# Kernel tuning notes

Measured on AMD Instinct MI355X. Metric: run time of the kernel, lower is better.

## Reference

```python
import jax, jax.numpy as jnp
import numpy as np

D_MODEL = 512
NUM_HEADS = 8
NUM_REL_EMB = 1024


def _linear(x, w, b):
    # torch nn.Linear convention: w is [out, in]
    return x @ w.T + b


def setup_inputs() -> dict:
    key = jax.random.key(0)
    B, S, D = 1, 512, D_MODEL
    ks = jax.random.split(key, 14)
    scale = D ** -0.5
    def w(i):
        return jax.random.normal(ks[i], (D, D), jnp.float32) * scale
    def b(i):
        return jax.random.normal(ks[i], (D,), jnp.float32) * 0.01
    return {
        "hidden_states": jax.random.normal(ks[0], (B, S, D), jnp.float32),
        "emb_table": jax.random.normal(ks[1], (NUM_REL_EMB, D), jnp.float32) * 0.02,
        "wq": w(2), "bq": b(3),
        "wk": w(4), "bk": b(5),
        "wv": w(6), "bv": b(7),
        "wrk": w(8), "brk": b(9),
        "wrq": w(10), "brq": b(11),
        "wo": w(12), "bo": b(13),
    }


def reference(hidden_states, emb_table, wq, bq, wk, bk, wv, bv,
              wrk, brk, wrq, brq, wo, bo):
    B, S, D = hidden_states.shape
    H = NUM_HEADS
    hd = D // H
    NE = emb_table.shape[0]

    # relative positions j - i, shifted and clamped, then embedded: [S, S, D]
    rel_pos = jnp.arange(S)[None, :] - jnp.arange(S)[:, None]
    idx = jnp.clip(rel_pos + NE // 2, 0, NE - 1)
    rel_emb = emb_table[idx]  # [S, S, D] (identical across batch)

    q = _linear(hidden_states, wq, bq).reshape(B, S, H, hd).transpose(0, 2, 1, 3)  # [B,H,S,hd]
    k = _linear(hidden_states, wk, bk).reshape(B, S, H, hd).transpose(0, 2, 1, 3)
    v = _linear(hidden_states, wv, bv).reshape(B, S, H, hd).transpose(0, 2, 1, 3)

    rk = _linear(rel_emb, wrk, brk).reshape(S, S, H, hd)  # [i, j, H, hd]
    rq = _linear(rel_emb, wrq, brq).reshape(S, S, H, hd)

    # content-content + content-relative + relative-content scores: [B,H,S,S]
    scores = (
        jnp.einsum('bhid,bhjd->bhij', q, k)
        + jnp.einsum('bhid,ijhd->bhij', q, rk)
        + jnp.einsum('ijhd,bhjd->bhij', rq, k)
    )

    attn = jax.nn.softmax(scores / jnp.sqrt(jnp.asarray(hd, scores.dtype)), axis=-1)
    # dropout is identity (p=0.0 / eval mode)

    ctx = jnp.einsum('bhij,bhjd->bhid', attn, v)          # [B,H,S,hd]
    ctx = ctx.transpose(0, 2, 1, 3).reshape(B, S, D)       # merge heads
    out = _linear(ctx, wo, bo)
    return out, attn
```

## Files before the change

### kernel.cpp

```cpp
#include <hip/hip_runtime.h>
#include <stdint.h>


typedef __bf16 bf16_t;
typedef bf16_t bf16x8 __attribute__((ext_vector_type(8)));
typedef float f32x4 __attribute__((ext_vector_type(4)));

__device__ __forceinline__ uint16_t f2bf(float f) {
  union { float f; uint32_t i; } c; c.f = f;
  return (uint16_t)((c.i + 0x7fffu + ((c.i >> 16) & 1u)) >> 16);
}
__device__ __forceinline__ uint32_t pack2bf(float lo, float hi) {
  return (uint32_t)f2bf(lo) | ((uint32_t)f2bf(hi) << 16);
}
#define MFMA(a, b, c) __builtin_amdgcn_mfma_f32_16x16x32_bf16((a), (b), (c), 0, 0, 0)

#define LSTR 40
#define SSTR 72

__global__ __launch_bounds__(256) void gemm_bt_kernel(
    const void* __restrict__ A, int lda, int zsA, int aF32,
    const void* __restrict__ B, int ldb, int zsB, int bF32,
    const float* __restrict__ bias, int hasBias,
    float* __restrict__ C, int ldc, int zsC, int K)
{
  __shared__ __align__(16) uint16_t As[64 * LSTR];
  __shared__ __align__(16) uint16_t Bs[64 * LSTR];
  const int z = blockIdx.z;
  const int m0 = blockIdx.y * 64, n0 = blockIdx.x * 64;
  const int t = threadIdx.x, lane = t & 63, wave = t >> 6;
  const int wi = wave & 1, wj = wave >> 1;
  const int quad = lane >> 4, l15 = lane & 15;
  const int srow = t >> 2, scol = (t & 3) * 8;

  f32x4 acc[2][2] = {};
  for (int k0 = 0; k0 < K; k0 += 32) {
    uint4 ap, bp;
    if (aF32) {
      const float* Af = (const float*)A + (size_t)z * zsA + (size_t)(m0 + srow) * lda + (k0 + scol);
      float4 x0 = *(const float4*)(Af); float4 x1 = *(const float4*)(Af + 4);
      ap.x = pack2bf(x0.x, x0.y); ap.y = pack2bf(x0.z, x0.w);
      ap.z = pack2bf(x1.x, x1.y); ap.w = pack2bf(x1.z, x1.w);
    } else {
      ap = *(const uint4*)((const uint16_t*)A + (size_t)z * zsA + (size_t)(m0 + srow) * lda + (k0 + scol));
    }
    if (bF32) {
      const float* Bf = (const float*)B + (size_t)z * zsB + (size_t)(n0 + srow) * ldb + (k0 + scol);
      float4 x0 = *(const float4*)(Bf); float4 x1 = *(const float4*)(Bf + 4);
      bp.x = pack2bf(x0.x, x0.y); bp.y = pack2bf(x0.z, x0.w);
      bp.z = pack2bf(x1.x, x1.y); bp.w = pack2bf(x1.z, x1.w);
    } else {
      bp = *(const uint4*)((const uint16_t*)B + (size_t)z * zsB + (size_t)(n0 + srow) * ldb + (k0 + scol));
    }
    *(uint4*)(&As[srow * LSTR + scol]) = ap;
    *(uint4*)(&Bs[srow * LSTR + scol]) = bp;
    __syncthreads();
    bf16x8 af[2], bfr[2];
#pragma unroll
    for (int x = 0; x < 2; x++) {
      af[x]  = *(const bf16x8*)(&As[(wi * 32 + x * 16 + l15) * LSTR + quad * 8]);
      bfr[x] = *(const bf16x8*)(&Bs[(wj * 32 + x * 16 + l15) * LSTR + quad * 8]);
    }
#pragma unroll
    for (int x = 0; x < 2; x++)
#pragma unroll
      for (int y = 0; y < 2; y++)
        acc[x][y] = MFMA(af[x], bfr[y], acc[x][y]);
    __syncthreads();
  }
#pragma unroll
  for (int x = 0; x < 2; x++)
#pragma unroll
    for (int y = 0; y < 2; y++) {
      const int j = n0 + wj * 32 + y * 16 + l15;
      const float bval = hasBias ? bias[j] : 0.0f;
      const int ib = m0 + wi * 32 + x * 16 + quad * 4;
#pragma unroll
      for (int r = 0; r < 4; r++)
        C[(size_t)z * zsC + (size_t)(ib + r) * ldc + j] = acc[x][y][r] + bval;
    }
}

__global__ __launch_bounds__(256) void proj_kernel(
    const float* __restrict__ X, const float* __restrict__ emb,
    const float* __restrict__ wq, const float* __restrict__ bq,
    const float* __restrict__ wk, const float* __restrict__ bk,
    const float* __restrict__ wv, const float* __restrict__ bv,
    const float* __restrict__ wrk, const float* __restrict__ brk,
    const float* __restrict__ wrq, const float* __restrict__ brq,
    uint16_t* __restrict__ q, uint16_t* __restrict__ k, uint16_t* __restrict__ vT,
    uint16_t* __restrict__ rkE, uint16_t* __restrict__ rqE)
{
  int bid = blockIdx.x;
  const float *A, *B, *bias; uint16_t* C; int mode;
  if (bid < 64)       {            A = X;   B = wq;  bias = bq;  C = q;   mode = 2; }
  else if (bid < 128) { bid -= 64; A = X;   B = wk;  bias = bk;  C = k;   mode = 2; }
  else if (bid < 192) { bid -= 128; A = X;  B = wv;  bias = bv;  C = vT;  mode = 3; }
  else if (bid < 320) { bid -= 192; A = emb; B = wrk; bias = brk; C = rkE; mode = 1; }
  else                { bid -= 320; A = emb; B = wrq; bias = brq; C = rqE; mode = 1; }
  const int m0 = (bid >> 3) * 64, n0 = (bid & 7) * 64;

  __shared__ __align__(16) uint16_t As[64 * LSTR];
  __shared__ __align__(16) uint16_t Bs[64 * LSTR];
  const int t = threadIdx.x, lane = t & 63, wave = t >> 6;
  const int wi = wave & 1, wj = wave >> 1;
  const int quad = lane >> 4, l15 = lane & 15;
  const int srow = t >> 2, scol = (t & 3) * 8;

  f32x4 acc[2][2] = {};
  for (int k0 = 0; k0 < 512; k0 += 32) {
    const float* Af = A + (size_t)(m0 + srow) * 512 + (k0 + scol);
    const float* Bf = B + (size_t)(n0 + srow) * 512 + (k0 + scol);
    float4 a0 = *(const float4*)(Af), a1 = *(const float4*)(Af + 4);
    float4 b0 = *(const float4*)(Bf), b1 = *(const float4*)(Bf + 4);
    uint4 ap, bp;
    ap.x = pack2bf(a0.x, a0.y); ap.y = pack2bf(a0.z, a0.w);
    ap.z = pack2bf(a1.x, a1.y); ap.w = pack2bf(a1.z, a1.w);
    bp.x = pack2bf(b0.x, b0.y); bp.y = pack2bf(b0.z, b0.w);
    bp.z = pack2bf(b1.x, b1.y); bp.w = pack2bf(b1.z, b1.w);
    *(uint4*)(&As[srow * LSTR + scol]) = ap;
    *(uint4*)(&Bs[srow * LSTR + scol]) = bp;
    __syncthreads();
    bf16x8 af[2], bfr[2];
#pragma unroll
    for (int x = 0; x < 2; x++) {
      af[x]  = *(const bf16x8*)(&As[(wi * 32 + x * 16 + l15) * LSTR + quad * 8]);
      bfr[x] = *(const bf16x8*)(&Bs[(wj * 32 + x * 16 + l15) * LSTR + quad * 8]);
    }
#pragma unroll
    for (int x = 0; x < 2; x++)
#pragma unroll
      for (int y = 0; y < 2; y++)
        acc[x][y] = MFMA(af[x], bfr[y], acc[x][y]);
    __syncthreads();
  }
#pragma unroll
  for (int x = 0; x < 2; x++)
#pragma unroll
    for (int y = 0; y < 2; y++) {
      const int j = n0 + wj * 32 + y * 16 + l15;
      const float bval = bias[j];
      const int ib = m0 + wi * 32 + x * 16 + quad * 4;
#pragma unroll
      for (int r = 0; r < 4; r++) {
        const int i = ib + r;
        size_t off;
        if (mode == 1)      off = (size_t)i * 512 + j;
        else if (mode == 2) off = (size_t)(j >> 6) * 32768 + (size_t)i * 64 + (size_t)(j & 63);
        else                off = (size_t)(j >> 6) * 32768 + (size_t)(j & 63) * 512 + (size_t)i;
        C[off] = f2bf(acc[x][y][r] + bval);
      }
    }
}

__global__ __launch_bounds__(256, 1) void attn_fused_kernel(
    const uint16_t* __restrict__ q, const uint16_t* __restrict__ k,
    const uint16_t* __restrict__ rkE, const uint16_t* __restrict__ rqE,
    const uint16_t* __restrict__ vT,
    float* __restrict__ attn, uint16_t* __restrict__ ctx_bf)
{
  __shared__ __align__(16) char smem[131840];
  const int h = blockIdx.y, i0 = blockIdx.x * 16;
  const int t = threadIdx.x, lane = t & 63, w = t >> 6;
  const int quad = lane >> 4, l15 = lane & 15;

  uint16_t* stgw = (uint16_t*)smem + w * 16128;
  float* U2f  = (float*)stgw;
  float* U3f  = (float*)((char*)stgw + 5376);
  uint16_t* Pw = stgw;
  float* ctxw = (float*)((char*)stgw + 8192);
  uint16_t* qs = (uint16_t*)(smem + 129024);
  float* rmax = (float*)(smem + 131328);
  float* rsum = rmax + 64;

  if (t < 128) {
    const int row = t >> 3, col = (t & 7) * 8;
    *(uint4*)(&qs[row * SSTR + col]) =
        *(const uint4*)(q + (size_t)h * 32768 + (size_t)(i0 + row) * 64 + col);
  }

  f32x4 sc[2][4];
  const int jbase = w * 2;
#pragma unroll
  for (int jt2 = 0; jt2 < 2; jt2++) {
    const int j0 = (jbase + jt2) * 64;
    const int ebase = j0 - i0 + 497;
    __syncthreads();
#pragma unroll
    for (int c = 0; c < 28; c++) {
      const int idx = lane + c * 64;
      const int row = idx >> 3, col = (idx & 7) * 8;
      const uint16_t* src;
      if (row < 64)       src = k   + (size_t)h * 32768 + (size_t)(j0 + row) * 64 + col;
      else if (row < 144) src = rqE + (size_t)min(ebase + row - 64, 1023) * 512 + h * 64 + col;
      else                src = rkE + (size_t)min(ebase + row - 144, 1023) * 512 + h * 64 + col;
      *(uint4*)(&stgw[row * SSTR + col]) = *(const uint4*)src;
    }
    __syncthreads();

    f32x4 acc1[4] = {}, acc2[5] = {}, acc3[5][4] = {};
#pragma unroll
    for (int s = 0; s < 2; s++) {
      const int ko = s * 32 + quad * 8;
      bf16x8 aq = *(const bf16x8*)(&qs[l15 * SSTR + ko]);
      bf16x8 bk[4], arq[5], brk[5];
#pragma unroll
      for (int tt = 0; tt < 4; tt++) bk[tt]  = *(const bf16x8*)(&stgw[(tt * 16 + l15) * SSTR + ko]);
#pragma unroll
      for (int x = 0; x < 5; x++)    arq[x]  = *(const bf16x8*)(&stgw[(64 + x * 16 + l15) * SSTR + ko]);
#pragma unroll
      for (int x = 0; x < 5; x++)    brk[x]  = *(const bf16x8*)(&stgw[(144 + x * 16 + l15) * SSTR + ko]);
#pragma unroll
      for (int tt = 0; tt < 4; tt++) acc1[tt] = MFMA(aq, bk[tt], acc1[tt]);
#pragma unroll
      for (int x = 0; x < 5; x++)    acc2[x] = MFMA(aq, brk[x], acc2[x]);
#pragma unroll
      for (int x = 0; x < 5; x++)
#pragma unroll
        for (int tt = 0; tt < 4; tt++) acc3[x][tt] = MFMA(arq[x], bk[tt], acc3[x][tt]);
    }
    __syncthreads();
#pragma unroll
    for (int x = 0; x < 5; x++)
#pragma unroll
      for (int r = 0; r < 4; r++)
        U2f[(quad * 4 + r) * 84 + x * 16 + l15] = acc2[x][r];
#pragma unroll
    for (int x = 0; x < 5; x++)
#pragma unroll
      for (int tt = 0; tt < 4; tt++)
#pragma unroll
        for (int r = 0; r < 4; r++)
          U3f[(x * 16 + quad * 4 + r) * 68 + tt * 16 + l15] = acc3[x][tt][r];
    __syncthreads();
#pragma unroll
    for (int tt = 0; tt < 4; tt++)
#pragma unroll
      for (int r = 0; r < 4; r++) {
        const int ii = quad * 4 + r, jj = tt * 16 + l15;
        const int rb = jj - ii + 15;
        sc[jt2][tt][r] = (acc1[tt][r] + U2f[ii * 84 + rb] + U3f[rb * 68 + jj]) * 0.125f;
      }
  }

  float mrow[4], srow[4];
#pragma unroll
  for (int r = 0; r < 4; r++) {
    float m = -1e30f;
#pragma unroll
    for (int jt2 = 0; jt2 < 2; jt2++)
#pragma unroll
      for (int tt = 0; tt < 4; tt++) m = fmaxf(m, sc[jt2][tt][r]);
#pragma unroll
    for (int o = 1; o < 16; o <<= 1) m = fmaxf(m, __shfl_xor(m, o, 64));
    mrow[r] = m;
  }
  if (l15 == 0)
#pragma unroll
    for (int r = 0; r < 4; r++) rmax[w * 16 + quad * 4 + r] = mrow[r];
  __syncthreads();
#pragma unroll
  for (int r = 0; r < 4; r++) {
    const int row = quad * 4 + r;
    const float m = fmaxf(fmaxf(rmax[row], rmax[16 + row]), fmaxf(rmax[32 + row], rmax[48 + row]));
    float s = 0.f;
#pragma unroll
    for (int jt2 = 0; jt2 < 2; jt2++)
#pragma unroll
      for (int tt = 0; tt < 4; tt++) {
        const float p = __expf(sc[jt2][tt][r] - m);
        sc[jt2][tt][r] = p; s += p;
      }
#pragma unroll
    for (int o = 1; o < 16; o <<= 1) s += __shfl_xor(s, o, 64);
    srow[r] = s;
  }
  if (l15 == 0)
#pragma unroll
    for (int r = 0; r < 4; r++) rsum[w * 16 + quad * 4 + r] = srow[r];
  __syncthreads();
#pragma unroll
  for (int r = 0; r < 4; r++) {
    const int row = quad * 4 + r;
    const float inv = 1.0f / (rsum[row] + rsum[16 + row] + rsum[32 + row] + rsum[48 + row]);
#pragma unroll
    for (int jt2 = 0; jt2 < 2; jt2++)
#pragma unroll
      for (int tt = 0; tt < 4; tt++) {
        sc[jt2][tt][r] *= inv;
        attn[((size_t)h * 512 + i0 + row) * 512 + (jbase + jt2) * 64 + tt * 16 + l15]
            = sc[jt2][tt][r];
      }
  }

  f32x4 apv[4] = {};
#pragma unroll
  for (int jt2 = 0; jt2 < 2; jt2++) {
    __syncthreads();
#pragma unroll
    for (int tt = 0; tt < 4; tt++)
#pragma unroll
      for (int r = 0; r < 4; r++)
        Pw[(quad * 4 + r) * SSTR + tt * 16 + l15] = f2bf(sc[jt2][tt][r]);
    __syncthreads();
#pragma unroll
    for (int s = 0; s < 2; s++) {
      const int ko = s * 32 + quad * 8;
      bf16x8 aP = *(const bf16x8*)(&Pw[l15 * SSTR + ko]);
#pragma unroll
      for (int tt = 0; tt < 4; tt++) {
        bf16x8 bv = *(const bf16x8*)(vT + (size_t)h * 32768 + (size_t)(tt * 16 + l15) * 512
                                     + (jbase + jt2) * 64 + ko);
        apv[tt] = MFMA(aP, bv, apv[tt]);
      }
    }
  }
#pragma unroll
  for (int tt = 0; tt < 4; tt++)
#pragma unroll
    for (int r = 0; r < 4; r++)
      ctxw[(quad * 4 + r) * 64 + tt * 16 + l15] = apv[tt][r];
  __syncthreads();
  {
    const int row = t >> 4, col = (t & 15) * 4;
    const size_t off = (size_t)(row * 64 + col) * 4;
    float4 s0 = *(const float4*)(smem + 0 * 32256 + 8192 + off);
    float4 s1 = *(const float4*)(smem + 1 * 32256 + 8192 + off);
    float4 s2 = *(const float4*)(smem + 2 * 32256 + 8192 + off);
    float4 s3 = *(const float4*)(smem + 3 * 32256 + 8192 + off);
    const float c0 = s0.x + s1.x + s2.x + s3.x;
    const float c1 = s0.y + s1.y + s2.y + s3.y;
    const float c2 = s0.z + s1.z + s2.z + s3.z;
    const float c3 = s0.w + s1.w + s2.w + s3.w;
    uint2 pk; pk.x = pack2bf(c0, c1); pk.y = pack2bf(c2, c3);
    *(uint2*)(ctx_bf + (size_t)(i0 + row) * 512 + h * 64 + col) = pk;
  }
}

extern "C" void kernel_launch(void* const* d_in, const int* in_sizes, int n_in,
                              void* d_out, int out_size, void* d_ws, size_t ws_size,
                              hipStream_t stream) {
  const float* X   = (const float*)d_in[0];
  const float* emb = (const float*)d_in[1];
  const float* wq  = (const float*)d_in[2];
  const float* bq  = (const float*)d_in[3];
  const float* wk  = (const float*)d_in[4];
  const float* bk  = (const float*)d_in[5];
  const float* wv  = (const float*)d_in[6];
  const float* bv  = (const float*)d_in[7];
  const float* wrk = (const float*)d_in[8];
  const float* brk = (const float*)d_in[9];
  const float* wrq = (const float*)d_in[10];
  const float* brq = (const float*)d_in[11];
  const float* wo  = (const float*)d_in[12];
  const float* bo  = (const float*)d_in[13];

  uint16_t* q      = (uint16_t*)d_ws;
  uint16_t* k      = q   + 262144;
  uint16_t* vT     = k   + 262144;
  uint16_t* rkE    = vT  + 262144;
  uint16_t* rqE    = rkE + 524288;
  uint16_t* ctx_bf = rqE + 524288;

  float* outp = (float*)d_out;
  float* attn = (float*)d_out + 262144;

  const dim3 blk(256);
  proj_kernel<<<dim3(448), blk, 0, stream>>>(X, emb, wq, bq, wk, bk, wv, bv,
                                             wrk, brk, wrq, brq, q, k, vT, rkE, rqE);
  attn_fused_kernel<<<dim3(32, 8), blk, 0, stream>>>(q, k, rkE, rqE, vT, attn, ctx_bf);
  gemm_bt_kernel<<<dim3(8, 8, 1), blk, 0, stream>>>(ctx_bf, 512, 0, 0,
                                                    wo, 512, 0, 1,
                                                    bo, 1, outp, 512, 0, 512);
}
```

Before: 131.0 us.

## Fuse output projection into attention kernel via per-head atomic accumulation

Removes the separate output-projection GEMM launch. Each attention block now multiplies its 16x64 per-head context tile by the matching slice of wo inside the kernel and atomically adds the partial result into the output. The output is pre-filled with the bias in the projection kernel. This saves one launch and the ctx round trip through global memory, at the cost of fp32 atomics from 8 heads per element, re-reading and converting wo from fp32 in every block, and a nondeterministic summation order.

```diff
diff --git a/kernel.cpp b/kernel.cpp
--- a/kernel.cpp
+++ b/kernel.cpp
@@ -17,69 +17,6 @@
 
 #define LSTR 40
 #define SSTR 72
-
-__global__ __launch_bounds__(256) void gemm_bt_kernel(
-    const void* __restrict__ A, int lda, int zsA, int aF32,
-    const void* __restrict__ B, int ldb, int zsB, int bF32,
-    const float* __restrict__ bias, int hasBias,
-    float* __restrict__ C, int ldc, int zsC, int K)
-{
-  __shared__ __align__(16) uint16_t As[64 * LSTR];
-  __shared__ __align__(16) uint16_t Bs[64 * LSTR];
-  const int z = blockIdx.z;
-  const int m0 = blockIdx.y * 64, n0 = blockIdx.x * 64;
-  const int t = threadIdx.x, lane = t & 63, wave = t >> 6;
-  const int wi = wave & 1, wj = wave >> 1;
-  const int quad = lane >> 4, l15 = lane & 15;
-  const int srow = t >> 2, scol = (t & 3) * 8;
-
-  f32x4 acc[2][2] = {};
-  for (int k0 = 0; k0 < K; k0 += 32) {
-    uint4 ap, bp;
-    if (aF32) {
-      const float* Af = (const float*)A + (size_t)z * zsA + (size_t)(m0 + srow) * lda + (k0 + scol);
-      float4 x0 = *(const float4*)(Af); float4 x1 = *(const float4*)(Af + 4);
-      ap.x = pack2bf(x0.x, x0.y); ap.y = pack2bf(x0.z, x0.w);
-      ap.z = pack2bf(x1.x, x1.y); ap.w = pack2bf(x1.z, x1.w);
-    } else {
-      ap = *(const uint4*)((const uint16_t*)A + (size_t)z * zsA + (size_t)(m0 + srow) * lda + (k0 + scol));
-    }
-    if (bF32) {
-      const float* Bf = (const float*)B + (size_t)z * zsB + (size_t)(n0 + srow) * ldb + (k0 + scol);
-      float4 x0 = *(const float4*)(Bf); float4 x1 = *(const float4*)(Bf + 4);
-      bp.x = pack2bf(x0.x, x0.y); bp.y = pack2bf(x0.z, x0.w);
-      bp.z = pack2bf(x1.x, x1.y); bp.w = pack2bf(x1.z, x1.w);
-    } else {
-      bp = *(const uint4*)((const uint16_t*)B + (size_t)z * zsB + (size_t)(n0 + srow) * ldb + (k0 + scol));
-    }
-    *(uint4*)(&As[srow * LSTR + scol]) = ap;
-    *(uint4*)(&Bs[srow * LSTR + scol]) = bp;
-    __syncthreads();
-    bf16x8 af[2], bfr[2];
-#pragma unroll
-    for (int x = 0; x < 2; x++) {
-      af[x]  = *(const bf16x8*)(&As[(wi * 32 + x * 16 + l15) * LSTR + quad * 8]);
-      bfr[x] = *(const bf16x8*)(&Bs[(wj * 32 + x * 16 + l15) * LSTR + quad * 8]);
-    }
-#pragma unroll
-    for (int x = 0; x < 2; x++)
-#pragma unroll
-      for (int y = 0; y < 2; y++)
-        acc[x][y] = MFMA(af[x], bfr[y], acc[x][y]);
-    __syncthreads();
-  }
-#pragma unroll
-  for (int x = 0; x < 2; x++)
-#pragma unroll
-    for (int y = 0; y < 2; y++) {
-      const int j = n0 + wj * 32 + y * 16 + l15;
-      const float bval = hasBias ? bias[j] : 0.0f;
-      const int ib = m0 + wi * 32 + x * 16 + quad * 4;
-#pragma unroll
-      for (int r = 0; r < 4; r++)
-        C[(size_t)z * zsC + (size_t)(ib + r) * ldc + j] = acc[x][y][r] + bval;
-    }
-}
 
 __global__ __launch_bounds__(256) void proj_kernel(
     const float* __restrict__ X, const float* __restrict__ emb,
@@ -88,10 +25,18 @@
     const float* __restrict__ wv, const float* __restrict__ bv,
     const float* __restrict__ wrk, const float* __restrict__ brk,
     const float* __restrict__ wrq, const float* __restrict__ brq,
+    const float* __restrict__ bo, float* __restrict__ outp,
     uint16_t* __restrict__ q, uint16_t* __restrict__ k, uint16_t* __restrict__ vT,
     uint16_t* __restrict__ rkE, uint16_t* __restrict__ rqE)
 {
+  const int t = threadIdx.x;
   int bid = blockIdx.x;
+  if (blockIdx.x < 64) {
+    for (int idx = t; idx < 8 * 512; idx += 256) {
+      const int row = blockIdx.x * 8 + (idx >> 9), col = idx & 511;
+      outp[(size_t)row * 512 + col] = bo[col];
+    }
+  }
   const float *A, *B, *bias; uint16_t* C; int mode;
   if (bid < 64)       {            A = X;   B = wq;  bias = bq;  C = q;   mode = 2; }
   else if (bid < 128) { bid -= 64; A = X;   B = wk;  bias = bk;  C = k;   mode = 2; }
@@ -102,7 +47,7 @@
 
   __shared__ __align__(16) uint16_t As[64 * LSTR];
   __shared__ __align__(16) uint16_t Bs[64 * LSTR];
-  const int t = threadIdx.x, lane = t & 63, wave = t >> 6;
+  const int lane = t & 63, wave = t >> 6;
   const int wi = wave & 1, wj = wave >> 1;
   const int quad = lane >> 4, l15 = lane & 15;
   const int srow = t >> 2, scol = (t & 3) * 8;
@@ -156,8 +101,8 @@
 __global__ __launch_bounds__(256, 1) void attn_fused_kernel(
     const uint16_t* __restrict__ q, const uint16_t* __restrict__ k,
     const uint16_t* __restrict__ rkE, const uint16_t* __restrict__ rqE,
-    const uint16_t* __restrict__ vT,
-    float* __restrict__ attn, uint16_t* __restrict__ ctx_bf)
+    const uint16_t* __restrict__ vT, const float* __restrict__ wo,
+    float* __restrict__ attn, float* __restrict__ outp)
 {
   __shared__ __align__(16) char smem[131840];
   const int h = blockIdx.y, i0 = blockIdx.x * 16;
@@ -170,6 +115,7 @@
   uint16_t* Pw = stgw;
   float* ctxw = (float*)((char*)stgw + 8192);
   uint16_t* qs = (uint16_t*)(smem + 129024);
+  uint16_t* ctxs = qs;
   float* rmax = (float*)(smem + 131328);
   float* rsum = rmax + 64;
 
@@ -328,13 +274,35 @@
     float4 s1 = *(const float4*)(smem + 1 * 32256 + 8192 + off);
     float4 s2 = *(const float4*)(smem + 2 * 32256 + 8192 + off);
     float4 s3 = *(const float4*)(smem + 3 * 32256 + 8192 + off);
-    const float c0 = s0.x + s1.x + s2.x + s3.x;
-    const float c1 = s0.y + s1.y + s2.y + s3.y;
-    const float c2 = s0.z + s1.z + s2.z + s3.z;
-    const float c3 = s0.w + s1.w + s2.w + s3.w;
-    uint2 pk; pk.x = pack2bf(c0, c1); pk.y = pack2bf(c2, c3);
-    *(uint2*)(ctx_bf + (size_t)(i0 + row) * 512 + h * 64 + col) = pk;
-  }
+    uint2 pk;
+    pk.x = pack2bf(s0.x + s1.x + s2.x + s3.x, s0.y + s1.y + s2.y + s3.y);
+    pk.y = pack2bf(s0.z + s1.z + s2.z + s3.z, s0.w + s1.w + s2.w + s3.w);
+    *(uint2*)(&ctxs[row * SSTR + col]) = pk;
+  }
+  __syncthreads();
+
+  f32x4 ao[8] = {};
+#pragma unroll
+  for (int s = 0; s < 2; s++) {
+    const int ko = s * 32 + quad * 8;
+    bf16x8 aC = *(const bf16x8*)(&ctxs[l15 * SSTR + ko]);
+#pragma unroll
+    for (int tt = 0; tt < 8; tt++) {
+      const int n = w * 128 + tt * 16 + l15;
+      const float* wrow = wo + (size_t)n * 512 + h * 64 + ko;
+      float4 x0 = *(const float4*)wrow, x1 = *(const float4*)(wrow + 4);
+      uint4 bwp;
+      bwp.x = pack2bf(x0.x, x0.y); bwp.y = pack2bf(x0.z, x0.w);
+      bwp.z = pack2bf(x1.x, x1.y); bwp.w = pack2bf(x1.z, x1.w);
+      ao[tt] = MFMA(*(bf16x8*)&bwp, aC, ao[tt]);
+    }
+  }
+#pragma unroll
+  for (int tt = 0; tt < 8; tt++)
+#pragma unroll
+    for (int r = 0; r < 4; r++)
+      atomicAdd(&outp[(size_t)(i0 + l15) * 512 + w * 128 + tt * 16 + quad * 4 + r],
+                ao[tt][r]);
 }
 
 extern "C" void kernel_launch(void* const* d_in, const int* in_sizes, int n_in,
@@ -355,21 +323,19 @@
   const float* wo  = (const float*)d_in[12];
   const float* bo  = (const float*)d_in[13];
 
-  uint16_t* q      = (uint16_t*)d_ws;
-  uint16_t* k      = q   + 262144;
-  uint16_t* vT     = k   + 262144;
-  uint16_t* rkE    = vT  + 262144;
-  uint16_t* rqE    = rkE + 524288;
-  uint16_t* ctx_bf = rqE + 524288;
+  uint16_t* q    = (uint16_t*)d_ws;
+  uint16_t* k    = q   + 262144;
+  uint16_t* vT   = k   + 262144;
+  uint16_t* rkE  = vT  + 262144;
+  uint16_t* rqE  = rkE + 524288;
 
   float* outp = (float*)d_out;
   float* attn = (float*)d_out + 262144;
 
   const dim3 blk(256);
   proj_kernel<<<dim3(448), blk, 0, stream>>>(X, emb, wq, bq, wk, bk, wv, bv,
-                                             wrk, brk, wrq, brq, q, k, vT, rkE, rqE);
-  attn_fused_kernel<<<dim3(32, 8), blk, 0, stream>>>(q, k, rkE, rqE, vT, attn, ctx_bf);
-  gemm_bt_kernel<<<dim3(8, 8, 1), blk, 0, stream>>>(ctx_bf, 512, 0, 0,
-                                                    wo, 512, 0, 1,
-                                                    bo, 1, outp, 512, 0, 512);
-}
+                                             wrk, brk, wrq, brq, bo, outp,
+                                             q, k, vT, rkE, rqE);
+  attn_fused_kernel<<<dim3(32, 8), blk, 0, stream>>>(q, k, rkE, rqE, vT, wo,
+                                                     attn, outp);
+}
```

Measured after the change: 146.9 us. 12.1% more time.
